# Performance work log

Hardware: AMD Instinct MI355X
Metric: run time of the kernel (lower is better)

Reference implementation:

```python
import jax, jax.numpy as jnp
import numpy as np
import math

# dims (match init_kwargs / input_specs)
T, B, S = 2048, 8, 512
D, H, DFF, NQ, W = 512, 8, 2048, 10, 16
EPS = 1e-5
NEG = -1e30


def _ln(x, g, b):
    mu = jnp.mean(x, axis=-1, keepdims=True)
    var = jnp.mean((x - mu) ** 2, axis=-1, keepdims=True)
    return (x - mu) * jax.lax.rsqrt(var + EPS) * g + b


def setup_inputs() -> dict:
    key = jax.random.key(0)
    ks = jax.random.split(key, 10)
    f = lambda k, shape, s=0.02: jax.random.normal(k, shape, jnp.float32) * s
    return {
        'tgt': jax.random.normal(ks[0], (T, B, D), jnp.float32),
        'memory': jax.random.normal(ks[1], (S, B, D), jnp.float32),
        'queries': f(ks[2], (NQ, D), 1.0 / math.sqrt(D)),
        'wk': f(ks[3], (NQ, 1), 1.0 / math.sqrt(NQ)),
        'in_proj_w': f(ks[4], (3 * D, D)),
        'in_proj_b': jnp.zeros((3 * D,), jnp.float32),
        'out_proj_w': f(ks[5], (D, D)),
        'out_proj_b': jnp.zeros((D,), jnp.float32),
        'lin1_w': f(ks[6], (DFF, D)),
        'lin1_b': jnp.zeros((DFF,), jnp.float32),
        'lin2_w': f(ks[7], (D, DFF)),
        'lin2_b': jnp.zeros((D,), jnp.float32),
        'ln1_g': jnp.ones((D,), jnp.float32), 'ln1_b': jnp.zeros((D,), jnp.float32),
        'ln2_g': jnp.ones((D,), jnp.float32), 'ln2_b': jnp.zeros((D,), jnp.float32),
        'ln3_g': jnp.ones((D,), jnp.float32), 'ln3_b': jnp.zeros((D,), jnp.float32),
    }


def _qa_block(x, queries, wk):
    # x: (T, B, D). Learned queries: per-head unit-norm + depth scale (QaN).
    dh = D // H
    q = queries.reshape(NQ, H, dh)
    q = q / (jnp.linalg.norm(q, axis=-1, keepdims=True) + 1e-6)
    q = (q / math.sqrt(dh)).reshape(NQ, D)
    # LocalAttention(window=W, look_backward=1, look_forward=1, non-causal, autopad)
    # k = v = x; T % W == 0 so autopad is a no-op.
    xb = jnp.transpose(x, (1, 0, 2))                       # (B, T, D)
    nw = T // W
    scale = D ** -0.5                                      # dim_head = D (single-head local attn)
    bk = xb.reshape(B, nw, W, D)
    pad = jnp.zeros((B, 1, W, D), x.dtype)
    bkp = jnp.concatenate([pad, bk, pad], axis=1)          # (B, nw+2, W, D)
    kv = jnp.concatenate([bkp[:, i:i + nw] for i in range(3)], axis=2)  # (B, nw, 3W, D)
    win_ok = jnp.pad(jnp.ones((nw,), bool), (1, 1))
    vm = jnp.stack([win_ok[i:i + nw] for i in range(3)], axis=1)        # (nw, 3)
    kmask = jnp.repeat(vm, W, axis=1)                                   # (nw, 3W)
    # The query vector is identical for every time step, so every position in a
    # window sees the same (query, keyset) pair -> one attention row per (n, window).
    sim = jnp.einsum('nd,bmjd->bnmj', q * scale, kv)       # (B, NQ, nw, 3W)
    sim = jnp.where(kmask[None, None], sim, NEG)
    attn = jax.nn.softmax(sim, axis=-1)
    out = jnp.einsum('bnmj,bmjd->bnmd', attn, kv)          # (B, NQ, nw, D)
    out = jnp.einsum('bnmd,n->bmd', out, wk[:, 0])         # mix N queries via wk (N,1)
    out = jnp.broadcast_to(out[:, :, None], (B, nw, W, D)).reshape(B, T, D)
    return jnp.transpose(out, (1, 0, 2))                   # (T, B, D)


def _mha_block(x, mem, in_w, in_b, out_w, out_b):
    dh = D // H
    wq, wkk, wv = jnp.split(in_w, 3, axis=0)
    bq, bk, bv = jnp.split(in_b, 3)
    q = (x @ wq.T + bq).reshape(T, B, H, dh).transpose(1, 2, 0, 3)   # (B,H,T,dh)
    k = (mem @ wkk.T + bk).reshape(S, B, H, dh).transpose(1, 2, 0, 3)
    v = (mem @ wv.T + bv).reshape(S, B, H, dh).transpose(1, 2, 0, 3)
    attn = jax.nn.softmax(jnp.einsum('bhtd,bhsd->bhts', q, k) / math.sqrt(dh), axis=-1)
    o = jnp.einsum('bhts,bhsd->bhtd', attn, v).transpose(2, 0, 1, 3).reshape(T, B, D)
    return o @ out_w.T + out_b


def reference(tgt, memory, queries, wk, in_proj_w, in_proj_b, out_proj_w, out_proj_b,
              lin1_w, lin1_b, lin2_w, lin2_b, ln1_g, ln1_b, ln2_g, ln2_b, ln3_g, ln3_b):
    # post-norm (norm_first=False), eval mode: dropouts + stochastic_depth(rate=0) are identity
    x = tgt
    x = _ln(x + _qa_block(x, queries, wk), ln1_g, ln1_b)
    x = _ln(x + _mha_block(x, memory, in_proj_w, in_proj_b, out_proj_w, out_proj_b), ln2_g, ln2_b)
    ff = jax.nn.relu(x @ lin1_w.T + lin1_b) @ lin2_w.T + lin2_b
    x = _ln(x + ff, ln3_g, ln3_b)
    # x = tgt + stochastic_depth(x - tgt) == x in eval / rate 0
    return x
```

## Files before the change

### kernel.cpp

```cpp
#include <hip/hip_runtime.h>


typedef unsigned short u16;
typedef unsigned int u32;
typedef short short8_t __attribute__((ext_vector_type(8)));
typedef float f32x4 __attribute__((ext_vector_type(4)));

#define TT 2048
#define BB 8
#define SS 512
#define DD 512
#define HH 8
#define DH 64
#define DFF 2048
#define NQ 10
#define WW 16
#define NW 128
#define KVPART 2097152

__device__ __forceinline__ float b2f(u16 u) {
    return __uint_as_float(((unsigned int)u) << 16);
}
__device__ __forceinline__ u16 f2b(float f) {
    unsigned int x = __float_as_uint(f);
    unsigned int r = x + 0x7FFFu + ((x >> 16) & 1u);
    return (u16)(r >> 16);
}
__device__ __forceinline__ float wave_sum(float v) {
    #pragma unroll
    for (int o = 32; o > 0; o >>= 1) v += __shfl_xor(v, o, 64);
    return v;
}
__device__ __forceinline__ float wave_max(float v) {
    #pragma unroll
    for (int o = 32; o > 0; o >>= 1) v = fmaxf(v, __shfl_xor(v, o, 64));
    return v;
}
__device__ __forceinline__ void load4(const u16* p, float* v) {
    ushort4 t = *(const ushort4*)p;
    v[0] = b2f(t.x); v[1] = b2f(t.y); v[2] = b2f(t.z); v[3] = b2f(t.w);
}
__device__ __forceinline__ void load4(const float* p, float* v) {
    float4 t = *(const float4*)p;
    v[0] = t.x; v[1] = t.y; v[2] = t.z; v[3] = t.w;
}
__device__ __forceinline__ void st1(u16* p, float v) { *p = f2b(v); }
__device__ __forceinline__ void st1(float* p, float v) { *p = v; }

__device__ __forceinline__ void async16(const u16* g, u16* l) {
    __builtin_amdgcn_global_load_lds((const __attribute__((address_space(1))) u32*)g,
                                     (__attribute__((address_space(3))) u32*)l, 16, 0, 0);
}

__global__ __launch_bounds__(256) void cvt_kernel(const float* __restrict__ src,
                                                  u16* __restrict__ dst) {
    int i = (blockIdx.x * 256 + threadIdx.x) * 4;
    float4 v = *(const float4*)(src + i);
    ushort4 o;
    o.x = f2b(v.x); o.y = f2b(v.y); o.z = f2b(v.z); o.w = f2b(v.w);
    *(ushort4*)(dst + i) = o;
}

__global__ __launch_bounds__(512) void qeff_kernel(const float* __restrict__ queries,
                                                   float* __restrict__ qeff) {
    int d = threadIdx.x;
    const float KS = 0.0055242717280199026f;
    for (int n = 0; n < NQ; n++) {
        float v = queries[n * DD + d];
        float ss = wave_sum(v * v);
        float norm = sqrtf(ss);
        qeff[n * DD + d] = v / (norm + 1e-6f) * KS;
    }
}

__global__ __launch_bounds__(256) void p_kernel(const float* __restrict__ x,
                                                const float* __restrict__ qeff,
                                                float* __restrict__ p) {
    __shared__ float qe[NQ * DD];
    for (int i = threadIdx.x; i < NQ * DD; i += 256) qe[i] = qeff[i];
    __syncthreads();
    int b = blockIdx.x >> 9;
    int t = ((blockIdx.x & 511) << 2) + (threadIdx.x >> 6);
    int lane = threadIdx.x & 63;
    const float* xr = x + ((size_t)t * BB + b) * DD;
    float acc[NQ];
    #pragma unroll
    for (int n = 0; n < NQ; n++) acc[n] = 0.f;
    #pragma unroll
    for (int c = 0; c < 8; c++) {
        int d = c * 64 + lane;
        float xv = xr[d];
        #pragma unroll
        for (int n = 0; n < NQ; n++) acc[n] += xv * qe[n * DD + d];
    }
    #pragma unroll
    for (int n = 0; n < NQ; n++) {
        float s = wave_sum(acc[n]);
        if (lane == 0) p[((size_t)(b * NQ + n)) * TT + t] = s;
    }
}

__global__ __launch_bounds__(256) void win_kernel(const float* __restrict__ p,
                                                  const float* __restrict__ wk,
                                                  float* __restrict__ Acomb) {
    int id = blockIdx.x * 4 + (threadIdx.x >> 6);
    int b = id >> 7, m = id & 127;
    int j = threadIdx.x & 63;
    int tj = (m - 1) * WW + j;
    bool valid = (j < 48) && (tj >= 0) && (tj < TT);
    float acc = 0.f;
    for (int n = 0; n < NQ; n++) {
        float v = valid ? p[((size_t)(b * NQ + n)) * TT + tj] : -1e30f;
        float mx = wave_max(v);
        float e = valid ? __expf(v - mx) : 0.f;
        float s = wave_sum(e);
        acc += wk[n] * (e / s);
    }
    if (j < 48) Acomb[(size_t)id * 48 + j] = acc;
}

__global__ __launch_bounds__(256) void mix_kernel(const float* __restrict__ Acomb,
                                                  const float* __restrict__ x,
                                                  float* __restrict__ mixed) {
    __shared__ float As[48];
    int id = blockIdx.x;
    int b = id >> 7, m = id & 127;
    if (threadIdx.x < 48) As[threadIdx.x] = Acomb[(size_t)id * 48 + threadIdx.x];
    __syncthreads();
    int d0 = threadIdx.x, d1 = threadIdx.x + 256;
    float a0 = 0.f, a1 = 0.f;
    int tb = (m - 1) * WW;
    for (int j = 0; j < 48; j++) {
        int t = tb + j;
        if ((unsigned)t < (unsigned)TT) {
            float aj = As[j];
            const float* xr = x + ((size_t)t * BB + b) * DD;
            a0 += aj * xr[d0];
            a1 += aj * xr[d1];
        }
    }
    mixed[(size_t)id * DD + d0] = a0;
    mixed[(size_t)id * DD + d1] = a1;
}

__global__ __launch_bounds__(256) void ln_qa_kernel(const float* __restrict__ a,
                                                    const float* __restrict__ mixed,
                                                    const float* __restrict__ g,
                                                    const float* __restrict__ bt,
                                                    u16* __restrict__ out) {
    int r = blockIdx.x * 4 + (threadIdx.x >> 6);
    int lane = threadIdx.x & 63;
    int t = r >> 3, b = r & 7;
    const float* ar = a + (size_t)r * DD;
    const float* mr = mixed + ((size_t)(b * NW + (t >> 4))) * DD;
    int d0 = lane * 8;
    float av[8], mv[8], gg[8], bb[8];
    load4(ar + d0, av); load4(ar + d0 + 4, av + 4);
    load4(mr + d0, mv); load4(mr + d0 + 4, mv + 4);
    load4(g + d0, gg);  load4(g + d0 + 4, gg + 4);
    load4(bt + d0, bb); load4(bt + d0 + 4, bb + 4);
    float v[8];
    float s = 0.f, s2 = 0.f;
    #pragma unroll
    for (int u = 0; u < 8; u++) { v[u] = av[u] + mv[u]; s += v[u]; s2 += v[u] * v[u]; }
    s = wave_sum(s); s2 = wave_sum(s2);
    float mu = s * (1.f / DD);
    float var = s2 * (1.f / DD) - mu * mu;
    float rs = rsqrtf(var + 1e-5f);
    #pragma unroll
    for (int u = 0; u < 8; u++) out[(size_t)r * DD + d0 + u] = f2b((v[u] - mu) * rs * gg[u] + bb[u]);
}

template <typename OT>
__global__ __launch_bounds__(256) void ln_rows_kernel(const u16* __restrict__ a,
                                                      const u16* __restrict__ bsrc,
                                                      const float* __restrict__ g,
                                                      const float* __restrict__ bt,
                                                      OT* __restrict__ out) {
    int r = blockIdx.x * 4 + (threadIdx.x >> 6);
    int lane = threadIdx.x & 63;
    const u16* ar = a + (size_t)r * DD;
    const u16* br = bsrc + (size_t)r * DD;
    int d0 = lane * 8;
    float av[8], cv[8], gg[8], bb[8];
    load4(ar + d0, av); load4(ar + d0 + 4, av + 4);
    load4(br + d0, cv); load4(br + d0 + 4, cv + 4);
    load4(g + d0, gg);  load4(g + d0 + 4, gg + 4);
    load4(bt + d0, bb); load4(bt + d0 + 4, bb + 4);
    float v[8];
    float s = 0.f, s2 = 0.f;
    #pragma unroll
    for (int u = 0; u < 8; u++) { v[u] = av[u] + cv[u]; s += v[u]; s2 += v[u] * v[u]; }
    s = wave_sum(s); s2 = wave_sum(s2);
    float mu = s * (1.f / DD);
    float var = s2 * (1.f / DD) - mu * mu;
    float rs = rsqrtf(var + 1e-5f);
    #pragma unroll
    for (int u = 0; u < 8; u++) st1(out + (size_t)r * DD + d0 + u, (v[u] - mu) * rs * gg[u] + bb[u]);
}

template <int RELU, int MT, int KV>
__global__ __launch_bounds__(256) void gemm_lds(const u16* __restrict__ A,
                                                const u16* __restrict__ W,
                                                const float* __restrict__ bias,
                                                u16* __restrict__ C,
                                                int M, int N, int K) {
    constexpr int BM = MT * 32;
    constexpr int NIA = BM / 64;
    __shared__ u16 As[2][BM * 32];
    __shared__ u16 Bs[2][128 * 32];
    int tid = threadIdx.x;
    int w = tid >> 6, lane = tid & 63;
    int n16 = lane & 15, quad = lane >> 4;
    int m0 = blockIdx.y * BM, n0 = blockIdx.x * 128;
    int wm16 = (w >> 1) * MT;
    int wn = (w & 1) * 64;

    const u16* gA[NIA];
    u16* lA[NIA];
    #pragma unroll
    for (int i = 0; i < NIA; i++) {
        int s = (w * NIA + i) * 64 + lane;
        int mb = s >> 6, kseg = (s >> 4) & 3, m = s & 15;
        gA[i] = A + (size_t)(m0 + mb * 16 + m) * K + kseg * 8;
        lA[i] = &As[0][(size_t)((w * NIA + i) * 64) * 8];
    }
    const u16* gB[2];
    u16* lB[2];
    #pragma unroll
    for (int i = 0; i < 2; i++) {
        int s = (w * 2 + i) * 64 + lane;
        int nb = s >> 6, kseg = (s >> 4) & 3, n = s & 15;
        gB[i] = W + (size_t)(n0 + nb * 16 + n) * K + kseg * 8;
        lB[i] = &Bs[0][(size_t)((w * 2 + i) * 64) * 8];
    }

    f32x4 acc[MT][4];
    #pragma unroll
    for (int i = 0; i < MT; i++)
        #pragma unroll
        for (int j = 0; j < 4; j++) acc[i][j] = (f32x4){0.f, 0.f, 0.f, 0.f};

    const int nk = K >> 5;
    #pragma unroll
    for (int i = 0; i < NIA; i++) async16(gA[i], lA[i]);
    #pragma unroll
    for (int i = 0; i < 2; i++) async16(gB[i], lB[i]);
    __syncthreads();

    for (int t = 0; t < nk; t++) {
        int cur = t & 1;
        if (t + 1 < nk) {
            int nxt = cur ^ 1;
            #pragma unroll
            for (int i = 0; i < NIA; i++) async16(gA[i] + (t + 1) * 32, lA[i] + nxt * (BM * 32));
            #pragma unroll
            for (int i = 0; i < 2; i++) async16(gB[i] + (t + 1) * 32, lB[i] + nxt * 4096);
        }
        const u16* Ac = &As[cur][0];
        const u16* Bc = &Bs[cur][0];
        short8_t af[MT], bf[4];
        #pragma unroll
        for (int im = 0; im < MT; im++)
            af[im] = *(const short8_t*)(Ac + (size_t)((wm16 + im) * 64 + lane) * 8);
        #pragma unroll
        for (int in = 0; in < 4; in++)
            bf[in] = *(const short8_t*)(Bc + (size_t)(((w & 1) * 4 + in) * 64 + lane) * 8);
        #pragma unroll
        for (int im = 0; im < MT; im++)
            #pragma unroll
            for (int in = 0; in < 4; in++)
                acc[im][in] = __builtin_amdgcn_mfma_f32_16x16x32_bf16(af[im], bf[in], acc[im][in], 0, 0, 0);
        __syncthreads();
    }

    float bia[4];
    #pragma unroll
    for (int in = 0; in < 4; in++) bia[in] = bias[n0 + wn + in * 16 + n16];
    #pragma unroll
    for (int im = 0; im < MT; im++) {
        #pragma unroll
        for (int r = 0; r < 4; r++) {
            int row = m0 + (wm16 + im) * 16 + quad * 4 + r;
            #pragma unroll
            for (int in = 0; in < 4; in++) {
                float v = acc[im][in][r] + bia[in];
                if (RELU) v = fmaxf(v, 0.f);
                if (KV) {
                    int col = n0 + wn + in * 16 + n16;
                    int part = col >> 9, h = (col >> 6) & 7, d = col & 63;
                    int s = row >> 3, bq = row & 7;
                    C[(size_t)part * KVPART + ((size_t)(bq * HH + h) * SS + s) * DH + d] = f2b(v);
                } else {
                    C[(size_t)row * N + n0 + wn + in * 16 + n16] = f2b(v);
                }
            }
        }
    }
}

__global__ __launch_bounds__(256) void attn_wp(const u16* __restrict__ qb,
                                               const u16* __restrict__ kvb,
                                               u16* __restrict__ ob) {
    __shared__ u16 Kb[2][2048];
    __shared__ u16 Vt[2][64][40];
    __shared__ u16 Ps[4][16][40];
    int tid = threadIdx.x;
    int w = tid >> 6, lane = tid & 63;
    int n16 = lane & 15, quad = lane >> 4, q8 = quad * 8;
    int b = blockIdx.y >> 3, h = blockIdx.y & 7;
    int q0 = blockIdx.x * 64 + w * 16;

    const u16* qrow = qb + ((size_t)(q0 + n16) * BB + b) * DD + h * DH;
    short8_t aq0 = *(const short8_t*)(qrow + q8);
    short8_t aq1 = *(const short8_t*)(qrow + 32 + q8);

    const u16* kbase = kvb + (size_t)(b * HH + h) * (SS * DH);
    const u16* vbase = kvb + (size_t)KVPART + (size_t)(b * HH + h) * (SS * DH);

    const u16* gK = kbase + (size_t)((w >> 1) * 16 + n16) * DH + (w & 1) * 32 + q8;
    int kp2 = (lane & 15) * 2;
    int vd = w * 16 + quad * 4;
    const u16* gV = vbase + (size_t)kp2 * DH + vd;

    float lsum[4];
    f32x4 Oa[4];
    #pragma unroll
    for (int r = 0; r < 4; r++) lsum[r] = 0.f;
    #pragma unroll
    for (int ot = 0; ot < 4; ot++) Oa[ot] = (f32x4){0.f, 0.f, 0.f, 0.f};

    union VU { ushort4 q; u16 h[4]; };

    {
        async16(gK, &Kb[0][w * 512]);
        VU va, vb2;
        va.q  = *(const ushort4*)(gV);
        vb2.q = *(const ushort4*)(gV + DH);
        #pragma unroll
        for (int u = 0; u < 4; u++)
            *(u32*)&Vt[0][vd + u][kp2] = (u32)va.h[u] | ((u32)vb2.h[u] << 16);
    }
    __syncthreads();

    for (int c = 0; c < 16; c++) {
        int cur = c & 1, nxt = cur ^ 1;

        VU va, vb2;
        if (c < 15) {
            const u16* gVc = gV + (size_t)(c + 1) * 32 * DH;
            va.q  = *(const ushort4*)(gVc);
            vb2.q = *(const ushort4*)(gVc + DH);
            async16(gK + (size_t)(c + 1) * 32 * DH, &Kb[nxt][w * 512]);
        }

        f32x4 sc[2];
        #pragma unroll
        for (int nt = 0; nt < 2; nt++) {
            short8_t bk0 = *(const short8_t*)&Kb[cur][(nt * 2 + 0) * 512 + lane * 8];
            short8_t bk1 = *(const short8_t*)&Kb[cur][(nt * 2 + 1) * 512 + lane * 8];
            f32x4 a = (f32x4){0.f, 0.f, 0.f, 0.f};
            a = __builtin_amdgcn_mfma_f32_16x16x32_bf16(aq0, bk0, a, 0, 0, 0);
            a = __builtin_amdgcn_mfma_f32_16x16x32_bf16(aq1, bk1, a, 0, 0, 0);
            sc[nt] = a;
        }

        #pragma unroll
        for (int r = 0; r < 4; r++) {
            float p0 = __expf(sc[0][r] * 0.125f - 8.0f);
            float p1 = __expf(sc[1][r] * 0.125f - 8.0f);
            lsum[r] += p0 + p1;
            Ps[w][quad * 4 + r][n16] = f2b(p0);
            Ps[w][quad * 4 + r][16 + n16] = f2b(p1);
        }

        short8_t ap = *(const short8_t*)&Ps[w][n16][q8];
        #pragma unroll
        for (int ot = 0; ot < 4; ot++) {
            short8_t bv = *(const short8_t*)&Vt[cur][ot * 16 + n16][q8];
            Oa[ot] = __builtin_amdgcn_mfma_f32_16x16x32_bf16(ap, bv, Oa[ot], 0, 0, 0);
        }

        if (c < 15) {
            #pragma unroll
            for (int u = 0; u < 4; u++)
                *(u32*)&Vt[nxt][vd + u][kp2] = (u32)va.h[u] | ((u32)vb2.h[u] << 16);
        }
        __syncthreads();
    }

    #pragma unroll
    for (int r = 0; r < 4; r++) {
        float l = lsum[r];
        #pragma unroll
        for (int o = 1; o < 16; o <<= 1) l += __shfl_xor(l, o, 64);
        float inv = 1.f / l;
        int t = q0 + quad * 4 + r;
        u16* orow = ob + ((size_t)t * BB + b) * DD + h * DH + n16;
        #pragma unroll
        for (int ot = 0; ot < 4; ot++) orow[ot * 16] = f2b(Oa[ot][r] * inv);
    }
}

extern "C" void kernel_launch(void* const* d_in, const int* in_sizes, int n_in,
                              void* d_out, int out_size, void* d_ws, size_t ws_size,
                              hipStream_t stream) {
    const float* tgt       = (const float*)d_in[0];
    const float* memory    = (const float*)d_in[1];
    const float* queries   = (const float*)d_in[2];
    const float* wk        = (const float*)d_in[3];
    const float* in_proj_w = (const float*)d_in[4];
    const float* in_proj_b = (const float*)d_in[5];
    const float* out_proj_w= (const float*)d_in[6];
    const float* out_proj_b= (const float*)d_in[7];
    const float* lin1_w    = (const float*)d_in[8];
    const float* lin1_b    = (const float*)d_in[9];
    const float* lin2_w    = (const float*)d_in[10];
    const float* lin2_b    = (const float*)d_in[11];
    const float* ln1_g     = (const float*)d_in[12];
    const float* ln1_b     = (const float*)d_in[13];
    const float* ln2_g     = (const float*)d_in[14];
    const float* ln2_b     = (const float*)d_in[15];
    const float* ln3_g     = (const float*)d_in[16];
    const float* ln3_b     = (const float*)d_in[17];

    char* w = (char*)d_ws;
    float* qeff  = (float*)(w + 0);
    float* pbuf  = (float*)(w + 20480);
    float* Acomb = (float*)(w + 675840);
    float* mixed = (float*)(w + 872448);
    u16* y1  = (u16*)(w + 2969600);
    u16* qb  = (u16*)(w + 19746816);
    u16* kvb = (u16*)(w + 36524032);
    u16* ob  = (u16*)(w + 44912640);
    u16* ipwb = (u16*)(w + 44912640);
    u16* memb = (u16*)(w + 46485504);
    u16* opwb = (u16*)(w + 36524032);
    u16* l1wb = (u16*)(w + 37048320);
    u16* l2wb = (u16*)(w + 39145472);
    u16* t1 = qb;
    u16* y2 = ob;
    u16* hb = qb;
    u16* fb = y1;

    cvt_kernel<<<(SS * BB * DD) / 1024, 256, 0, stream>>>(memory, memb);
    cvt_kernel<<<(3 * DD * DD) / 1024, 256, 0, stream>>>(in_proj_w, ipwb);

    qeff_kernel<<<1, 512, 0, stream>>>(queries, qeff);
    p_kernel<<<BB * (TT / 4), 256, 0, stream>>>(tgt, qeff, pbuf);
    win_kernel<<<(BB * NW) / 4, 256, 0, stream>>>(pbuf, wk, Acomb);
    mix_kernel<<<BB * NW, 256, 0, stream>>>(Acomb, tgt, mixed);
    ln_qa_kernel<<<(TT * BB) / 4, 256, 0, stream>>>(tgt, mixed, ln1_g, ln1_b, y1);

    gemm_lds<0, 4, 0><<<dim3(DD / 128, (TT * BB) / 128), 256, 0, stream>>>(y1, ipwb, in_proj_b, qb, TT * BB, DD, DD);
    gemm_lds<0, 4, 1><<<dim3(1024 / 128, (SS * BB) / 128), 256, 0, stream>>>(memb, ipwb + (size_t)DD * DD, in_proj_b + DD, kvb, SS * BB, 1024, DD);
    attn_wp<<<dim3(TT / 64, BB * HH), 256, 0, stream>>>(qb, kvb, ob);
    cvt_kernel<<<(DD * DD) / 1024, 256, 0, stream>>>(out_proj_w, opwb);
    cvt_kernel<<<(DFF * DD) / 1024, 256, 0, stream>>>(lin1_w, l1wb);
    cvt_kernel<<<(DD * DFF) / 1024, 256, 0, stream>>>(lin2_w, l2wb);
    gemm_lds<0, 4, 0><<<dim3(DD / 128, (TT * BB) / 128), 256, 0, stream>>>(ob, opwb, out_proj_b, t1, TT * BB, DD, DD);
    ln_rows_kernel<u16><<<(TT * BB) / 4, 256, 0, stream>>>(y1, t1, ln2_g, ln2_b, y2);

    for (int c = 0; c < 4; c++) {
        const u16* y2c = y2 + (size_t)c * 4096 * DD;
        u16* fbc = fb + (size_t)c * 4096 * DD;
        gemm_lds<1, 4, 0><<<dim3(DFF / 128, 4096 / 128), 256, 0, stream>>>(y2c, l1wb, lin1_b, hb, 4096, DFF, DD);
        gemm_lds<0, 2, 0><<<dim3(DD / 128, 4096 / 64), 256, 0, stream>>>(hb, l2wb, lin2_b, fbc, 4096, DD, DFF);
    }
    ln_rows_kernel<float><<<(TT * BB) / 4, 256, 0, stream>>>(y2, fb, ln3_g, ln3_b, (float*)d_out);
}
```

Measured before the change: 565.7 us.

## Fuse conversions and window kernels, restructure cross-attention to keep P in registers

Merges the separate fp32-to-bf16 conversion launches into two combined kernels and fuses the window-softmax and mixing kernels into one. Reworks the cross-attention kernel so each wave handles 32 queries with transposed score MFMAs, which lets the probabilities be packed straight into MFMA operands with v_cvt_pk_bf16 instead of round-tripping through LDS. It also remaps blocks across XCDs and reorders the V key loading to match the new register layout. The goal is fewer launches and less LDS traffic in attention, at the cost of halving the attention grid size and more register pressure.

Result: faster. 538.6 us (-4.8%).

```diff
diff --git a/kernel.cpp b/kernel.cpp
--- a/kernel.cpp
+++ b/kernel.cpp
@@ -26,6 +26,11 @@
     unsigned int r = x + 0x7FFFu + ((x >> 16) & 1u);
     return (u16)(r >> 16);
 }
+__device__ __forceinline__ u32 cvt_pk_bf16(float lo, float hi) {
+    u32 r;
+    asm volatile("v_cvt_pk_bf16_f32 %0, %1, %2" : "=v"(r) : "v"(lo), "v"(hi));
+    return r;
+}
 __device__ __forceinline__ float wave_sum(float v) {
     #pragma unroll
     for (int o = 32; o > 0; o >>= 1) v += __shfl_xor(v, o, 64);
@@ -52,13 +57,41 @@
                                      (__attribute__((address_space(3))) u32*)l, 16, 0, 0);
 }
 
-__global__ __launch_bounds__(256) void cvt_kernel(const float* __restrict__ src,
-                                                  u16* __restrict__ dst) {
-    int i = (blockIdx.x * 256 + threadIdx.x) * 4;
-    float4 v = *(const float4*)(src + i);
+__device__ __forceinline__ void xcd_remap(int& bx, int& by) {
+    int flat = blockIdx.y * gridDim.x + blockIdx.x;
+    int xcd = flat & 7;
+    int j = flat >> 3;
+    by = xcd * ((int)gridDim.y >> 3) + j / (int)gridDim.x;
+    bx = j % (int)gridDim.x;
+}
+
+__device__ __forceinline__ void cvt_block(const float* s, u16* d, int base) {
+    int i = base + threadIdx.x * 4;
+    float4 v = *(const float4*)(s + i);
     ushort4 o;
     o.x = f2b(v.x); o.y = f2b(v.y); o.z = f2b(v.z); o.w = f2b(v.w);
-    *(ushort4*)(dst + i) = o;
+    *(ushort4*)(d + i) = o;
+}
+
+__global__ __launch_bounds__(256) void cvt2_kernel(const float* __restrict__ s0,
+                                                   const float* __restrict__ s1,
+                                                   u16* __restrict__ d0,
+                                                   u16* __restrict__ d1) {
+    int bid = blockIdx.x;
+    if (bid < 2048) cvt_block(s0, d0, bid * 1024);
+    else            cvt_block(s1, d1, (bid - 2048) * 1024);
+}
+
+__global__ __launch_bounds__(256) void cvt3_kernel(const float* __restrict__ s0,
+                                                   const float* __restrict__ s1,
+                                                   const float* __restrict__ s2,
+                                                   u16* __restrict__ d0,
+                                                   u16* __restrict__ d1,
+                                                   u16* __restrict__ d2) {
+    int bid = blockIdx.x;
+    if (bid < 256)       cvt_block(s0, d0, bid * 1024);
+    else if (bid < 1280) cvt_block(s1, d1, (bid - 256) * 1024);
+    else                 cvt_block(s2, d2, (bid - 1280) * 1024);
 }
 
 __global__ __launch_bounds__(512) void qeff_kernel(const float* __restrict__ queries,
@@ -100,32 +133,27 @@
     }
 }
 
-__global__ __launch_bounds__(256) void win_kernel(const float* __restrict__ p,
-                                                  const float* __restrict__ wk,
-                                                  float* __restrict__ Acomb) {
-    int id = blockIdx.x * 4 + (threadIdx.x >> 6);
-    int b = id >> 7, m = id & 127;
-    int j = threadIdx.x & 63;
-    int tj = (m - 1) * WW + j;
-    bool valid = (j < 48) && (tj >= 0) && (tj < TT);
-    float acc = 0.f;
-    for (int n = 0; n < NQ; n++) {
-        float v = valid ? p[((size_t)(b * NQ + n)) * TT + tj] : -1e30f;
-        float mx = wave_max(v);
-        float e = valid ? __expf(v - mx) : 0.f;
-        float s = wave_sum(e);
-        acc += wk[n] * (e / s);
-    }
-    if (j < 48) Acomb[(size_t)id * 48 + j] = acc;
-}
-
-__global__ __launch_bounds__(256) void mix_kernel(const float* __restrict__ Acomb,
-                                                  const float* __restrict__ x,
-                                                  float* __restrict__ mixed) {
+__global__ __launch_bounds__(256) void winmix_kernel(const float* __restrict__ p,
+                                                     const float* __restrict__ wk,
+                                                     const float* __restrict__ x,
+                                                     float* __restrict__ mixed) {
     __shared__ float As[48];
     int id = blockIdx.x;
     int b = id >> 7, m = id & 127;
-    if (threadIdx.x < 48) As[threadIdx.x] = Acomb[(size_t)id * 48 + threadIdx.x];
+    if (threadIdx.x < 64) {
+        int j = threadIdx.x;
+        int tj = (m - 1) * WW + j;
+        bool valid = (j < 48) && (tj >= 0) && (tj < TT);
+        float acc = 0.f;
+        for (int n = 0; n < NQ; n++) {
+            float v = valid ? p[((size_t)(b * NQ + n)) * TT + tj] : -1e30f;
+            float mx = wave_max(v);
+            float e = valid ? __expf(v - mx) : 0.f;
+            float s = wave_sum(e);
+            acc += wk[n] * (e / s);
+        }
+        if (j < 48) As[j] = acc;
+    }
     __syncthreads();
     int d0 = threadIdx.x, d1 = threadIdx.x + 256;
     float a0 = 0.f, a1 = 0.f;
@@ -304,33 +332,43 @@
                                                u16* __restrict__ ob) {
     __shared__ u16 Kb[2][2048];
     __shared__ u16 Vt[2][64][40];
-    __shared__ u16 Ps[4][16][40];
     int tid = threadIdx.x;
     int w = tid >> 6, lane = tid & 63;
     int n16 = lane & 15, quad = lane >> 4, q8 = quad * 8;
-    int b = blockIdx.y >> 3, h = blockIdx.y & 7;
-    int q0 = blockIdx.x * 64 + w * 16;
-
-    const u16* qrow = qb + ((size_t)(q0 + n16) * BB + b) * DD + h * DH;
-    short8_t aq0 = *(const short8_t*)(qrow + q8);
-    short8_t aq1 = *(const short8_t*)(qrow + 32 + q8);
+    int xb, bh;
+    xcd_remap(xb, bh);
+    int b = bh >> 3, h = bh & 7;
+    int q0 = xb * 128 + w * 32;
+
+    short8_t aq[2][2];
+    #pragma unroll
+    for (int qt = 0; qt < 2; qt++) {
+        const u16* qrow = qb + ((size_t)(q0 + qt * 16 + n16) * BB + b) * DD + h * DH;
+        aq[qt][0] = *(const short8_t*)(qrow + q8);
+        aq[qt][1] = *(const short8_t*)(qrow + 32 + q8);
+    }
 
     const u16* kbase = kvb + (size_t)(b * HH + h) * (SS * DH);
     const u16* vbase = kvb + (size_t)KVPART + (size_t)(b * HH + h) * (SS * DH);
 
     const u16* gK = kbase + (size_t)((w >> 1) * 16 + n16) * DH + (w & 1) * 32 + q8;
-    int kp2 = (lane & 15) * 2;
+
+    int m = lane & 15;
+    int a2 = m >> 2, b2 = m & 3;
+    int key0 = (b2 < 2) ? (4 * a2 + 2 * b2) : (16 + 4 * a2 + 2 * (b2 - 2));
+    int kp2 = m * 2;
     int vd = w * 16 + quad * 4;
-    const u16* gV = vbase + (size_t)kp2 * DH + vd;
-
-    float lsum[4];
-    f32x4 Oa[4];
-    #pragma unroll
-    for (int r = 0; r < 4; r++) lsum[r] = 0.f;
-    #pragma unroll
-    for (int ot = 0; ot < 4; ot++) Oa[ot] = (f32x4){0.f, 0.f, 0.f, 0.f};
+    const u16* gV = vbase + (size_t)key0 * DH + vd;
+
+    float lsum[2] = {0.f, 0.f};
+    f32x4 Oa[2][4];
+    #pragma unroll
+    for (int qt = 0; qt < 2; qt++)
+        #pragma unroll
+        for (int ot = 0; ot < 4; ot++) Oa[qt][ot] = (f32x4){0.f, 0.f, 0.f, 0.f};
 
     union VU { ushort4 q; u16 h[4]; };
+    union PU { u32 wd[4]; short8_t s8; };
 
     {
         async16(gK, &Kb[0][w * 512]);
@@ -354,31 +392,41 @@
             async16(gK + (size_t)(c + 1) * 32 * DH, &Kb[nxt][w * 512]);
         }
 
-        f32x4 sc[2];
-        #pragma unroll
-        for (int nt = 0; nt < 2; nt++) {
-            short8_t bk0 = *(const short8_t*)&Kb[cur][(nt * 2 + 0) * 512 + lane * 8];
-            short8_t bk1 = *(const short8_t*)&Kb[cur][(nt * 2 + 1) * 512 + lane * 8];
-            f32x4 a = (f32x4){0.f, 0.f, 0.f, 0.f};
-            a = __builtin_amdgcn_mfma_f32_16x16x32_bf16(aq0, bk0, a, 0, 0, 0);
-            a = __builtin_amdgcn_mfma_f32_16x16x32_bf16(aq1, bk1, a, 0, 0, 0);
-            sc[nt] = a;
-        }
-
-        #pragma unroll
-        for (int r = 0; r < 4; r++) {
-            float p0 = __expf(sc[0][r] * 0.125f - 8.0f);
-            float p1 = __expf(sc[1][r] * 0.125f - 8.0f);
-            lsum[r] += p0 + p1;
-            Ps[w][quad * 4 + r][n16] = f2b(p0);
-            Ps[w][quad * 4 + r][16 + n16] = f2b(p1);
-        }
-
-        short8_t ap = *(const short8_t*)&Ps[w][n16][q8];
-        #pragma unroll
-        for (int ot = 0; ot < 4; ot++) {
-            short8_t bv = *(const short8_t*)&Vt[cur][ot * 16 + n16][q8];
-            Oa[ot] = __builtin_amdgcn_mfma_f32_16x16x32_bf16(ap, bv, Oa[ot], 0, 0, 0);
+        short8_t bk0 = *(const short8_t*)&Kb[cur][0 * 512 + lane * 8];
+        short8_t bk1 = *(const short8_t*)&Kb[cur][1 * 512 + lane * 8];
+        short8_t bk2 = *(const short8_t*)&Kb[cur][2 * 512 + lane * 8];
+        short8_t bk3 = *(const short8_t*)&Kb[cur][3 * 512 + lane * 8];
+
+        #pragma unroll
+        for (int qt = 0; qt < 2; qt++) {
+            f32x4 s0 = (f32x4){0.f, 0.f, 0.f, 0.f};
+            s0 = __builtin_amdgcn_mfma_f32_16x16x32_bf16(bk0, aq[qt][0], s0, 0, 0, 0);
+            s0 = __builtin_amdgcn_mfma_f32_16x16x32_bf16(bk1, aq[qt][1], s0, 0, 0, 0);
+            f32x4 s1 = (f32x4){0.f, 0.f, 0.f, 0.f};
+            s1 = __builtin_amdgcn_mfma_f32_16x16x32_bf16(bk2, aq[qt][0], s1, 0, 0, 0);
+            s1 = __builtin_amdgcn_mfma_f32_16x16x32_bf16(bk3, aq[qt][1], s1, 0, 0, 0);
+
+            float p0 = __expf(s0[0] * 0.125f - 8.0f);
+            float p1 = __expf(s0[1] * 0.125f - 8.0f);
+            float p2 = __expf(s0[2] * 0.125f - 8.0f);
+            float p3 = __expf(s0[3] * 0.125f - 8.0f);
+            float p4 = __expf(s1[0] * 0.125f - 8.0f);
+            float p5 = __expf(s1[1] * 0.125f - 8.0f);
+            float p6 = __expf(s1[2] * 0.125f - 8.0f);
+            float p7 = __expf(s1[3] * 0.125f - 8.0f);
+            lsum[qt] += ((p0 + p1) + (p2 + p3)) + ((p4 + p5) + (p6 + p7));
+
+            PU pu;
+            pu.wd[0] = cvt_pk_bf16(p0, p1);
+            pu.wd[1] = cvt_pk_bf16(p2, p3);
+            pu.wd[2] = cvt_pk_bf16(p4, p5);
+            pu.wd[3] = cvt_pk_bf16(p6, p7);
+
+            #pragma unroll
+            for (int ot = 0; ot < 4; ot++) {
+                short8_t bv = *(const short8_t*)&Vt[cur][ot * 16 + n16][q8];
+                Oa[qt][ot] = __builtin_amdgcn_mfma_f32_16x16x32_bf16(pu.s8, bv, Oa[qt][ot], 0, 0, 0);
+            }
         }
 
         if (c < 15) {
@@ -390,15 +438,19 @@
     }
 
     #pragma unroll
-    for (int r = 0; r < 4; r++) {
-        float l = lsum[r];
-        #pragma unroll
-        for (int o = 1; o < 16; o <<= 1) l += __shfl_xor(l, o, 64);
-        float inv = 1.f / l;
-        int t = q0 + quad * 4 + r;
-        u16* orow = ob + ((size_t)t * BB + b) * DD + h * DH + n16;
-        #pragma unroll
-        for (int ot = 0; ot < 4; ot++) orow[ot * 16] = f2b(Oa[ot][r] * inv);
+    for (int qt = 0; qt < 2; qt++) {
+        float l = lsum[qt];
+        l += __shfl_xor(l, 16, 64);
+        l += __shfl_xor(l, 32, 64);
+        #pragma unroll
+        for (int r = 0; r < 4; r++) {
+            float lq = __shfl(l, quad * 4 + r, 64);
+            float inv = 1.f / lq;
+            int t = q0 + qt * 16 + quad * 4 + r;
+            u16* orow = ob + ((size_t)t * BB + b) * DD + h * DH + n16;
+            #pragma unroll
+            for (int ot = 0; ot < 4; ot++) orow[ot * 16] = f2b(Oa[qt][ot][r] * inv);
+        }
     }
 }
 
@@ -427,7 +479,6 @@
     char* w = (char*)d_ws;
     float* qeff  = (float*)(w + 0);
     float* pbuf  = (float*)(w + 20480);
-    float* Acomb = (float*)(w + 675840);
     float* mixed = (float*)(w + 872448);
     u16* y1  = (u16*)(w + 2969600);
     u16* qb  = (u16*)(w + 19746816);
@@ -443,21 +494,17 @@
     u16* hb = qb;
     u16* fb = y1;
 
-    cvt_kernel<<<(SS * BB * DD) / 1024, 256, 0, stream>>>(memory, memb);
-    cvt_kernel<<<(3 * DD * DD) / 1024, 256, 0, stream>>>(in_proj_w, ipwb);
+    cvt2_kernel<<<2816, 256, 0, stream>>>(memory, in_proj_w, memb, ipwb);
 
     qeff_kernel<<<1, 512, 0, stream>>>(queries, qeff);
     p_kernel<<<BB * (TT / 4), 256, 0, stream>>>(tgt, qeff, pbuf);
-    win_kernel<<<(BB * NW) / 4, 256, 0, stream>>>(pbuf, wk, Acomb);
-    mix_kernel<<<BB * NW, 256, 0, stream>>>(Acomb, tgt, mixed);
+    winmix_kernel<<<BB * NW, 256, 0, stream>>>(pbuf, wk, tgt, mixed);
     ln_qa_kernel<<<(TT * BB) / 4, 256, 0, stream>>>(tgt, mixed, ln1_g, ln1_b, y1);
 
     gemm_lds<0, 4, 0><<<dim3(DD / 128, (TT * BB) / 128), 256, 0, stream>>>(y1, ipwb, in_proj_b, qb, TT * BB, DD, DD);
     gemm_lds<0, 4, 1><<<dim3(1024 / 128, (SS * BB) / 128), 256, 0, stream>>>(memb, ipwb + (size_t)DD * DD, in_proj_b + DD, kvb, SS * BB, 1024, DD);
-    attn_wp<<<dim3(TT / 64, BB * HH), 256, 0, stream>>>(qb, kvb, ob);
-    cvt_kernel<<<(DD * DD) / 1024, 256, 0, stream>>>(out_proj_w, opwb);
-    cvt_kernel<<<(DFF * DD) / 1024, 256, 0, stream>>>(lin1_w, l1wb);
-    cvt_kernel<<<(DD * DFF) / 1024, 256, 0, stream>>>(lin2_w, l2wb);
+    attn_wp<<<dim3(TT / 128, BB * HH), 256, 0, stream>>>(qb, kvb, ob);
+    cvt3_kernel<<<2304, 256, 0, stream>>>(out_proj_w, lin1_w, lin2_w, opwb, l1wb, l2wb);
     gemm_lds<0, 4, 0><<<dim3(DD / 128, (TT * BB) / 128), 256, 0, stream>>>(ob, opwb, out_proj_b, t1, TT * BB, DD, DD);
     ln_rows_kernel<u16><<<(TT * BB) / 4, 256, 0, stream>>>(y1, t1, ln2_g, ln2_b, y2);
 
```
